# Performance work log

Measured on AMD Instinct MI355X. Metric: run time of the kernel, lower is better.

Reference implementation:

```python
import jax, jax.numpy as jnp
import numpy as np

RADIUS = [1.0, 1.5, 2.0, 100.0]  # bucket boundaries; last is catch-all
NFILT = len(RADIUS)
C_IN, C_OUT = 256, 512


def setup_inputs() -> dict:
    key = jax.random.key(0)
    k1, k2, k3, k4 = jax.random.split(key, 4)
    b, n = 16, 4096
    feat = jax.random.normal(k1, (b, n, C_IN), dtype=jnp.float32)
    xyz = jax.random.normal(k2, (b, n, 3), dtype=jnp.float32)
    # init per original reset_parameters
    std = 2.0 * np.sqrt(2.0 / (C_IN + C_OUT))
    a = np.sqrt(3.0) * std
    weight = jax.random.uniform(k3, (NFILT, C_OUT, C_IN), dtype=jnp.float32, minval=-a, maxval=a)
    bound = 1.0 / np.sqrt(C_IN)
    bias = jax.random.uniform(k4, (NFILT, C_OUT), dtype=jnp.float32, minval=-bound, maxval=bound)
    return {"feat": feat, "xyz": xyz, "weight": weight, "bias": bias}


def reference(feat, xyz, weight, bias):
    b, n, c = feat.shape
    p = feat.reshape(b * n, c)                      # (P, C)
    radii = jnp.asarray(RADIUS, dtype=feat.dtype)
    r_norm = jnp.linalg.norm(xyz.reshape(b * n, 3), axis=1)
    # first radius with r_norm < r (same as the sequential break in map2filtId)
    filt_id = jnp.argmax(r_norm[:, None] < radii[None, :], axis=1)  # (P,)
    # grouped linear expressed densely: all Nfilt GEMMs, then per-point select
    all_out = jnp.einsum('pc,foc->fpo', p, weight) + bias[:, None, :]  # (F, P, O)
    out = jnp.take_along_axis(all_out, filt_id[None, :, None], axis=0)[0]  # (P, O)
    return out.reshape(b, n, -1)
```

## Files before the change

### kernel.cpp

```cpp
#include <hip/hip_runtime.h>
#include <hip/hip_bf16.h>

#define C_IN   256
#define C_OUT  512
#define NFILT  4

#define BM  128
#define SAS 264

typedef __attribute__((ext_vector_type(8))) short bf16x8;
typedef __attribute__((ext_vector_type(4))) float floatx4;
typedef __attribute__((ext_vector_type(4))) float f4v;

union Pack8 { uint4 u; __hip_bfloat16 h[8]; };

__global__ void zero_cnt_kernel(int* __restrict__ cnt) {
    if (threadIdx.x < NFILT) cnt[threadIdx.x] = 0;
}

__global__ void bucketize_kernel(const float* __restrict__ xyz,
                                 int* __restrict__ idxbuf,
                                 int* __restrict__ cnt, int P) {
    int pid = blockIdx.x * blockDim.x + threadIdx.x;
    if (pid >= P) return;
    float x = xyz[pid * 3 + 0];
    float y = xyz[pid * 3 + 1];
    float z = xyz[pid * 3 + 2];
    float r2 = __fadd_rn(__fadd_rn(__fmul_rn(x, x), __fmul_rn(y, y)), __fmul_rn(z, z));
    float r = sqrtf(r2);
    int filt;
    if (r < 1.0f)        filt = 0;
    else if (r < 1.5f)   filt = 1;
    else if (r < 2.0f)   filt = 2;
    else if (r < 100.0f) filt = 3;
    else                 filt = 0;

    int lane = threadIdx.x & 63;
    for (int f = 0; f < NFILT; ++f) {
        unsigned long long mask = __ballot(filt == f);
        if (mask == 0ull) continue;
        int leader = __ffsll((unsigned long long)mask) - 1;
        int base = 0;
        if (lane == leader) base = atomicAdd(&cnt[f], __popcll(mask));
        base = __shfl(base, leader);
        if (filt == f) {
            int off = __popcll(mask & ((1ull << lane) - 1ull));
            idxbuf[f * P + base + off] = pid;
        }
    }
}

__global__ void convert_w_kernel(const float* __restrict__ w,
                                 ushort* __restrict__ wbt) {
    int t = blockIdx.x * blockDim.x + threadIdx.x;
    int c8 = t & 31;
    int fo = t >> 5;
    int f  = fo >> 9;
    int o  = fo & 511;
    const float* src = w + (size_t)fo * C_IN + c8 * 8;
    f4v v0 = *(const f4v*)(src + 0);
    f4v v1 = *(const f4v*)(src + 4);
    Pack8 p;
    p.h[0] = __float2bfloat16(v0.x); p.h[1] = __float2bfloat16(v0.y);
    p.h[2] = __float2bfloat16(v0.z); p.h[3] = __float2bfloat16(v0.w);
    p.h[4] = __float2bfloat16(v1.x); p.h[5] = __float2bfloat16(v1.y);
    p.h[6] = __float2bfloat16(v1.z); p.h[7] = __float2bfloat16(v1.w);
    *(uint4*)(wbt + ((size_t)(f * 32 + c8) * 512 + o) * 8) = p.u;
}

__global__ __launch_bounds__(256, 2) void gemm_kernel(
    const float* __restrict__ feat, const ushort* __restrict__ wbt,
    const float* __restrict__ bias, const int* __restrict__ idxbuf,
    const int* __restrict__ cnt, float* __restrict__ out, int P)
{
    __shared__ ushort sA[BM * SAS];
    __shared__ float  sBias[C_OUT];
    __shared__ int    sIdx[BM];

    int t = blockIdx.x;
    int f = -1, lt = 0, cn = 0;
    for (int ff = 0; ff < NFILT; ++ff) {
        int c = cnt[ff];
        int nt = (c + BM - 1) / BM;
        if (t < nt) { f = ff; lt = t; cn = c; break; }
        t -= nt;
    }
    if (f < 0) return;

    int tid = threadIdx.x;
    int rowBase = lt * BM;
    if (tid < BM) {
        int r = rowBase + tid;
        sIdx[tid] = (r < cn) ? idxbuf[f * P + r] : -1;
    }
    sBias[tid]       = bias[f * C_OUT + tid];
    sBias[tid + 256] = bias[f * C_OUT + tid + 256];
    __syncthreads();

    int sRow = tid >> 1, sHalf = tid & 1;
    int myIdx = sIdx[sRow];
    const float* aRow = feat + (size_t)(myIdx < 0 ? 0 : myIdx) * C_IN + sHalf * 16;
    ushort* dA = &sA[sRow * SAS + sHalf * 16];
#pragma unroll
    for (int it = 0; it < 8; ++it) {
        const float* ap = aRow + it * 32;
        f4v a0 = __builtin_nontemporal_load((const f4v*)(ap + 0));
        f4v a1 = __builtin_nontemporal_load((const f4v*)(ap + 4));
        f4v a2 = __builtin_nontemporal_load((const f4v*)(ap + 8));
        f4v a3 = __builtin_nontemporal_load((const f4v*)(ap + 12));
        Pack8 p0, p1;
        p0.h[0] = __float2bfloat16(a0.x); p0.h[1] = __float2bfloat16(a0.y);
        p0.h[2] = __float2bfloat16(a0.z); p0.h[3] = __float2bfloat16(a0.w);
        p0.h[4] = __float2bfloat16(a1.x); p0.h[5] = __float2bfloat16(a1.y);
        p0.h[6] = __float2bfloat16(a1.z); p0.h[7] = __float2bfloat16(a1.w);
        p1.h[0] = __float2bfloat16(a2.x); p1.h[1] = __float2bfloat16(a2.y);
        p1.h[2] = __float2bfloat16(a2.z); p1.h[3] = __float2bfloat16(a2.w);
        p1.h[4] = __float2bfloat16(a3.x); p1.h[5] = __float2bfloat16(a3.y);
        p1.h[6] = __float2bfloat16(a3.z); p1.h[7] = __float2bfloat16(a3.w);
        *(uint4*)(dA + it * 32 + 0) = p0.u;
        *(uint4*)(dA + it * 32 + 8) = p1.u;
    }
    __syncthreads();

    int wid = tid >> 6, lane = tid & 63;
    int lcol = lane & 15, quad = lane >> 4;
    int rbase = wid * 32;
    int aOff0 = (rbase + lcol) * SAS + quad * 8;
    int aOff1 = aOff0 + 16 * SAS;

    int    pid_[2][4];
    size_t obase_[2][4];
#pragma unroll
    for (int i = 0; i < 2; ++i)
#pragma unroll
        for (int r = 0; r < 4; ++r) {
            int p_ = sIdx[rbase + i * 16 + quad * 4 + r];
            pid_[i][r]   = p_;
            obase_[i][r] = (size_t)(p_ < 0 ? 0 : p_) * C_OUT + lcol;
        }

    const ushort* bQuad = wbt + ((size_t)(f * 32 + quad) * 512 + lcol) * 8;

    for (int ot = 0; ot < 4; ++ot) {
        floatx4 acc[2][8];
#pragma unroll
        for (int i = 0; i < 2; ++i)
#pragma unroll
            for (int j = 0; j < 8; ++j)
                acc[i][j] = (floatx4){0.f, 0.f, 0.f, 0.f};

        const ushort* bOt = bQuad + (size_t)ot * 128 * 8;

        bf16x8 af[2][2], bfr[2][8];
        af[0][0] = *(const bf16x8*)&sA[aOff0];
        af[0][1] = *(const bf16x8*)&sA[aOff1];
#pragma unroll
        for (int j = 0; j < 8; ++j)
            bfr[0][j] = *(const bf16x8*)(bOt + j * 16 * 8);

#pragma unroll
        for (int kk = 0; kk < 8; ++kk) {
            int cur = kk & 1, nxt = cur ^ 1;
            if (kk < 7) {
                af[nxt][0] = *(const bf16x8*)&sA[aOff0 + (kk + 1) * 32];
                af[nxt][1] = *(const bf16x8*)&sA[aOff1 + (kk + 1) * 32];
                const ushort* bp = bOt + (size_t)(kk + 1) * 4 * 512 * 8;
#pragma unroll
                for (int j = 0; j < 8; ++j)
                    bfr[nxt][j] = *(const bf16x8*)(bp + j * 16 * 8);
            }
#pragma unroll
            for (int i = 0; i < 2; ++i)
#pragma unroll
                for (int j = 0; j < 8; ++j)
                    acc[i][j] = __builtin_amdgcn_mfma_f32_16x16x32_bf16(
                        af[cur][i], bfr[cur][j], acc[i][j], 0, 0, 0);
        }

#pragma unroll
        for (int j = 0; j < 8; ++j) {
            float bv = sBias[ot * 128 + j * 16 + lcol];
#pragma unroll
            for (int i = 0; i < 2; ++i)
#pragma unroll
                for (int r = 0; r < 4; ++r) {
                    if (pid_[i][r] >= 0)
                        __builtin_nontemporal_store(acc[i][j][r] + bv,
                            out + obase_[i][r] + ot * 128 + j * 16);
                }
        }
    }
}

extern "C" void kernel_launch(void* const* d_in, const int* in_sizes, int n_in,
                              void* d_out, int out_size, void* d_ws, size_t ws_size,
                              hipStream_t stream) {
    const float* feat = (const float*)d_in[0];
    const float* xyz  = (const float*)d_in[1];
    const float* w    = (const float*)d_in[2];
    const float* bias = (const float*)d_in[3];
    float* out = (float*)d_out;
    int P = in_sizes[0] / C_IN;

    char* ws = (char*)d_ws;
    int* idxbuf = (int*)ws;
    int* cntp   = (int*)(ws + (size_t)4 * P * 4);
    ushort* wbt = (ushort*)(ws + (size_t)4 * P * 4 + 16);

    zero_cnt_kernel<<<1, 64, 0, stream>>>(cntp);
    bucketize_kernel<<<(P + 255) / 256, 256, 0, stream>>>(xyz, idxbuf, cntp, P);
    convert_w_kernel<<<(NFILT * C_OUT * C_IN / 8 + 255) / 256, 256, 0, stream>>>(w, wbt);

    dim3 grid(P / BM + NFILT);
    gemm_kernel<<<grid, 256, 0, stream>>>(feat, wbt, bias, idxbuf, cntp, out, P);
}
```

Measured before the change: 285.8 us.

## Shrink row tile to 32 and split output columns across waves

The GEMM tile drops from 128 to 32 gathered rows per block. The four waves now each own a 128-column slice of the output instead of a 32-row slice, so each block computes its whole 32x512 tile in one pass rather than looping over four column tiles. The weight repack kernel writes a layout where each wave's B-fragment loads are contiguous 1KB reads, and launch bounds are raised to allow three blocks per CU. This aims to expose many more blocks and lower per-block LDS so latency is hidden better. In exchange, weights are re-read four times as often from L2, the register prefetch double-buffering is gone, and output stores are no longer nontemporal.

```diff
diff --git a/kernel.cpp b/kernel.cpp
--- a/kernel.cpp
+++ b/kernel.cpp
@@ -5,7 +5,7 @@
 #define C_OUT  512
 #define NFILT  4
 
-#define BM  128
+#define BM  32
 #define SAS 264
 
 typedef __attribute__((ext_vector_type(8))) short bf16x8;
@@ -57,6 +57,8 @@
     int fo = t >> 5;
     int f  = fo >> 9;
     int o  = fo & 511;
+    int ot = o >> 7, j = (o >> 4) & 7, lc = o & 15;
+    int kk = c8 >> 2, quad = c8 & 3;
     const float* src = w + (size_t)fo * C_IN + c8 * 8;
     f4v v0 = *(const f4v*)(src + 0);
     f4v v1 = *(const f4v*)(src + 4);
@@ -65,10 +67,11 @@
     p.h[2] = __float2bfloat16(v0.z); p.h[3] = __float2bfloat16(v0.w);
     p.h[4] = __float2bfloat16(v1.x); p.h[5] = __float2bfloat16(v1.y);
     p.h[6] = __float2bfloat16(v1.z); p.h[7] = __float2bfloat16(v1.w);
-    *(uint4*)(wbt + ((size_t)(f * 32 + c8) * 512 + o) * 8) = p.u;
-}
-
-__global__ __launch_bounds__(256, 2) void gemm_kernel(
+    size_t dst = (size_t)(f * 32 + ot * 8 + kk) * 4096 + j * 512 + (quad * 16 + lc) * 8;
+    *(uint4*)(wbt + dst) = p.u;
+}
+
+__global__ __launch_bounds__(256, 3) void gemm_kernel(
     const float* __restrict__ feat, const ushort* __restrict__ wbt,
     const float* __restrict__ bias, const int* __restrict__ idxbuf,
     const int* __restrict__ cnt, float* __restrict__ out, int P)
@@ -97,98 +100,81 @@
     sBias[tid + 256] = bias[f * C_OUT + tid + 256];
     __syncthreads();
 
-    int sRow = tid >> 1, sHalf = tid & 1;
-    int myIdx = sIdx[sRow];
-    const float* aRow = feat + (size_t)(myIdx < 0 ? 0 : myIdx) * C_IN + sHalf * 16;
-    ushort* dA = &sA[sRow * SAS + sHalf * 16];
-#pragma unroll
-    for (int it = 0; it < 8; ++it) {
-        const float* ap = aRow + it * 32;
-        f4v a0 = __builtin_nontemporal_load((const f4v*)(ap + 0));
-        f4v a1 = __builtin_nontemporal_load((const f4v*)(ap + 4));
-        f4v a2 = __builtin_nontemporal_load((const f4v*)(ap + 8));
-        f4v a3 = __builtin_nontemporal_load((const f4v*)(ap + 12));
-        Pack8 p0, p1;
-        p0.h[0] = __float2bfloat16(a0.x); p0.h[1] = __float2bfloat16(a0.y);
-        p0.h[2] = __float2bfloat16(a0.z); p0.h[3] = __float2bfloat16(a0.w);
-        p0.h[4] = __float2bfloat16(a1.x); p0.h[5] = __float2bfloat16(a1.y);
-        p0.h[6] = __float2bfloat16(a1.z); p0.h[7] = __float2bfloat16(a1.w);
-        p1.h[0] = __float2bfloat16(a2.x); p1.h[1] = __float2bfloat16(a2.y);
-        p1.h[2] = __float2bfloat16(a2.z); p1.h[3] = __float2bfloat16(a2.w);
-        p1.h[4] = __float2bfloat16(a3.x); p1.h[5] = __float2bfloat16(a3.y);
-        p1.h[6] = __float2bfloat16(a3.z); p1.h[7] = __float2bfloat16(a3.w);
-        *(uint4*)(dA + it * 32 + 0) = p0.u;
-        *(uint4*)(dA + it * 32 + 8) = p1.u;
+    {
+        int row = tid >> 3, c0 = (tid & 7) * 32;
+        int myIdx = sIdx[row];
+        const float* ap = feat + (size_t)(myIdx < 0 ? 0 : myIdx) * C_IN + c0;
+        ushort* dA = &sA[row * SAS + c0];
+#pragma unroll
+        for (int it = 0; it < 2; ++it) {
+            f4v a0 = __builtin_nontemporal_load((const f4v*)(ap + it * 16 + 0));
+            f4v a1 = __builtin_nontemporal_load((const f4v*)(ap + it * 16 + 4));
+            f4v a2 = __builtin_nontemporal_load((const f4v*)(ap + it * 16 + 8));
+            f4v a3 = __builtin_nontemporal_load((const f4v*)(ap + it * 16 + 12));
+            Pack8 p0, p1;
+            p0.h[0] = __float2bfloat16(a0.x); p0.h[1] = __float2bfloat16(a0.y);
+            p0.h[2] = __float2bfloat16(a0.z); p0.h[3] = __float2bfloat16(a0.w);
+            p0.h[4] = __float2bfloat16(a1.x); p0.h[5] = __float2bfloat16(a1.y);
+            p0.h[6] = __float2bfloat16(a1.z); p0.h[7] = __float2bfloat16(a1.w);
+            p1.h[0] = __float2bfloat16(a2.x); p1.h[1] = __float2bfloat16(a2.y);
+            p1.h[2] = __float2bfloat16(a2.z); p1.h[3] = __float2bfloat16(a2.w);
+            p1.h[4] = __float2bfloat16(a3.x); p1.h[5] = __float2bfloat16(a3.y);
+            p1.h[6] = __float2bfloat16(a3.z); p1.h[7] = __float2bfloat16(a3.w);
+            *(uint4*)(dA + it * 16 + 0) = p0.u;
+            *(uint4*)(dA + it * 16 + 8) = p1.u;
+        }
     }
     __syncthreads();
 
-    int wid = tid >> 6, lane = tid & 63;
+    int wOT  = tid >> 6;
+    int lane = tid & 63;
     int lcol = lane & 15, quad = lane >> 4;
-    int rbase = wid * 32;
-    int aOff0 = (rbase + lcol) * SAS + quad * 8;
-    int aOff1 = aOff0 + 16 * SAS;
-
-    int    pid_[2][4];
-    size_t obase_[2][4];
+
+    const ushort* bPtr = wbt + (size_t)(f * 32 + wOT * 8) * 4096
+                             + (size_t)(quad * 16 + lcol) * 8;
+    int aOff0 = lcol * SAS + quad * 8;
+    int aOff1 = (16 + lcol) * SAS + quad * 8;
+
+    floatx4 acc[2][8];
 #pragma unroll
     for (int i = 0; i < 2; ++i)
 #pragma unroll
-        for (int r = 0; r < 4; ++r) {
-            int p_ = sIdx[rbase + i * 16 + quad * 4 + r];
-            pid_[i][r]   = p_;
-            obase_[i][r] = (size_t)(p_ < 0 ? 0 : p_) * C_OUT + lcol;
+        for (int j = 0; j < 8; ++j)
+            acc[i][j] = (floatx4){0.f, 0.f, 0.f, 0.f};
+
+#pragma unroll
+    for (int kk = 0; kk < 8; ++kk) {
+        bf16x8 af0 = *(const bf16x8*)&sA[aOff0 + kk * 32];
+        bf16x8 af1 = *(const bf16x8*)&sA[aOff1 + kk * 32];
+        bf16x8 bfr[8];
+        const ushort* bk = bPtr + (size_t)kk * 4096;
+#pragma unroll
+        for (int j = 0; j < 8; ++j)
+            bfr[j] = *(const bf16x8*)(bk + j * 512);
+#pragma unroll
+        for (int j = 0; j < 8; ++j) {
+            acc[0][j] = __builtin_amdgcn_mfma_f32_16x16x32_bf16(af0, bfr[j], acc[0][j], 0, 0, 0);
+            acc[1][j] = __builtin_amdgcn_mfma_f32_16x16x32_bf16(af1, bfr[j], acc[1][j], 0, 0, 0);
         }
-
-    const ushort* bQuad = wbt + ((size_t)(f * 32 + quad) * 512 + lcol) * 8;
-
-    for (int ot = 0; ot < 4; ++ot) {
-        floatx4 acc[2][8];
+    }
+
+    int pid_[2][4];
+#pragma unroll
+    for (int i = 0; i < 2; ++i)
+#pragma unroll
+        for (int r = 0; r < 4; ++r)
+            pid_[i][r] = sIdx[i * 16 + quad * 4 + r];
+
+#pragma unroll
+    for (int j = 0; j < 8; ++j) {
+        int o = wOT * 128 + j * 16 + lcol;
+        float bv = sBias[o];
 #pragma unroll
         for (int i = 0; i < 2; ++i)
 #pragma unroll
-            for (int j = 0; j < 8; ++j)
-                acc[i][j] = (floatx4){0.f, 0.f, 0.f, 0.f};
-
-        const ushort* bOt = bQuad + (size_t)ot * 128 * 8;
-
-        bf16x8 af[2][2], bfr[2][8];
-        af[0][0] = *(const bf16x8*)&sA[aOff0];
-        af[0][1] = *(const bf16x8*)&sA[aOff1];
-#pragma unroll
-        for (int j = 0; j < 8; ++j)
-            bfr[0][j] = *(const bf16x8*)(bOt + j * 16 * 8);
-
-#pragma unroll
-        for (int kk = 0; kk < 8; ++kk) {
-            int cur = kk & 1, nxt = cur ^ 1;
-            if (kk < 7) {
-                af[nxt][0] = *(const bf16x8*)&sA[aOff0 + (kk + 1) * 32];
-                af[nxt][1] = *(const bf16x8*)&sA[aOff1 + (kk + 1) * 32];
-                const ushort* bp = bOt + (size_t)(kk + 1) * 4 * 512 * 8;
-#pragma unroll
-                for (int j = 0; j < 8; ++j)
-                    bfr[nxt][j] = *(const bf16x8*)(bp + j * 16 * 8);
-            }
-#pragma unroll
-            for (int i = 0; i < 2; ++i)
-#pragma unroll
-                for (int j = 0; j < 8; ++j)
-                    acc[i][j] = __builtin_amdgcn_mfma_f32_16x16x32_bf16(
-                        af[cur][i], bfr[cur][j], acc[i][j], 0, 0, 0);
-        }
-
-#pragma unroll
-        for (int j = 0; j < 8; ++j) {
-            float bv = sBias[ot * 128 + j * 16 + lcol];
-#pragma unroll
-            for (int i = 0; i < 2; ++i)
-#pragma unroll
-                for (int r = 0; r < 4; ++r) {
-                    if (pid_[i][r] >= 0)
-                        __builtin_nontemporal_store(acc[i][j][r] + bv,
-                            out + obase_[i][r] + ot * 128 + j * 16);
-                }
-        }
+            for (int r = 0; r < 4; ++r)
+                if (pid_[i][r] >= 0)
+                    out[(size_t)pid_[i][r] * C_OUT + o] = acc[i][j][r] + bv;
     }
 }
 
```

Result: no change. 285.9 us (+0.0%).
